# Performance work log

Hardware: AMD Instinct MI355X
Metric: run time of the kernel (lower is better)

## Reference

```python
import jax, jax.numpy as jnp
import numpy as np

N = 50000
E = 600000
HIDDEN = 128
HEADS = 4
HEAD_DIM = HIDDEN // HEADS
NEG_SLOPE = 0.2
LN_EPS = 1e-5


def setup_inputs() -> dict:
    key = jax.random.key(0)
    ks = jax.random.split(key, 16)
    s = 1.0 / np.sqrt(HIDDEN)
    inp = {
        "h": jax.random.normal(ks[0], (N, HIDDEN), dtype=jnp.float32),
        "src": jax.random.randint(ks[1], (E,), 0, N, dtype=jnp.int32),
        "dst": jax.random.randint(ks[2], (E,), 0, N, dtype=jnp.int32),
        # GATv2 params (share_weights=False, bias=True)
        "W_src": jax.random.normal(ks[3], (HIDDEN, HIDDEN), dtype=jnp.float32) * s,
        "b_src": jnp.zeros((HIDDEN,), dtype=jnp.float32),
        "W_dst": jax.random.normal(ks[4], (HIDDEN, HIDDEN), dtype=jnp.float32) * s,
        "b_dst": jnp.zeros((HIDDEN,), dtype=jnp.float32),
        "attn": jax.random.normal(ks[5], (HEADS, HEAD_DIM), dtype=jnp.float32) * s,
        # FFN params
        "W1": jax.random.normal(ks[6], (HIDDEN, 2 * HIDDEN), dtype=jnp.float32) * s,
        "bf1": jnp.zeros((2 * HIDDEN,), dtype=jnp.float32),
        "W2": jax.random.normal(ks[7], (2 * HIDDEN, HIDDEN), dtype=jnp.float32) * (1.0 / np.sqrt(2 * HIDDEN)),
        "bf2": jnp.zeros((HIDDEN,), dtype=jnp.float32),
        # LayerNorms
        "g1": jnp.ones((HIDDEN,), dtype=jnp.float32),
        "beta1": jnp.zeros((HIDDEN,), dtype=jnp.float32),
        "g2": jnp.ones((HIDDEN,), dtype=jnp.float32),
        "beta2": jnp.zeros((HIDDEN,), dtype=jnp.float32),
    }
    return inp


def _layernorm(x, g, b):
    mu = jnp.mean(x, axis=-1, keepdims=True)
    var = jnp.mean(jnp.square(x - mu), axis=-1, keepdims=True)
    return (x - mu) * jax.lax.rsqrt(var + LN_EPS) * g + b


def reference(h, src, dst, W_src, b_src, W_dst, b_dst, attn,
              W1, bf1, W2, bf2, g1, beta1, g2, beta2):
    # --- GATv2 attention (eval mode, dropouts are identity) ---
    fs = (h @ W_src + b_src).reshape(N, HEADS, HEAD_DIM)   # [N,H,D]
    fd = (h @ W_dst + b_dst).reshape(N, HEADS, HEAD_DIM)
    e = jax.nn.leaky_relu(fs[src] + fd[dst], NEG_SLOPE)    # [E,H,D]
    logits = jnp.einsum('ehd,hd->eh', e, attn)             # [E,H]
    # edge softmax over incoming edges of each dst node
    m = jax.ops.segment_max(logits, dst, num_segments=N)   # [N,H]
    m = jnp.where(jnp.isfinite(m), m, 0.0)                 # guard zero-in-degree
    a = jnp.exp(logits - m[dst])                           # [E,H]
    denom = jax.ops.segment_sum(a, dst, num_segments=N)    # [N,H]
    denom = jnp.where(denom == 0.0, 1.0, denom)
    alpha = a / denom[dst]                                 # [E,H]
    msg = fs[src] * alpha[:, :, None]                      # [E,H,D]
    rst = jax.ops.segment_sum(msg, dst, num_segments=N)    # [N,H,D]
    h_attn = rst.reshape(N, HIDDEN)
    # --- residual + LN, FFN + residual + LN ---
    h1 = _layernorm(h + h_attn, g1, beta1)
    ffn = jax.nn.gelu(h1 @ W1 + bf1, approximate=False) @ W2 + bf2
    out = _layernorm(h1 + ffn, g2, beta2)
    return out
```

## Files before the change

kernel.cpp:

```cpp
#include <hip/hip_runtime.h>
#include <math.h>

#define N_NODES 50000
#define N_EDGES 600000
#define HID 128
#define FFN_HID 256
#define NEG_SLOPE 0.2f
#define LN_EPS 1e-5f
#define BKT 64

typedef unsigned short u16;
typedef unsigned int u32;
typedef __attribute__((ext_vector_type(8))) short short8;
typedef __attribute__((ext_vector_type(4))) float floatx4;

__device__ __forceinline__ u16 f2bf(float x) {
    unsigned int u = __float_as_uint(x);
    unsigned int r = u + 0x7FFFu + ((u >> 16) & 1u);
    return (u16)(r >> 16);
}
__device__ __forceinline__ float bflo(u32 u) { return __uint_as_float(u << 16); }
__device__ __forceinline__ float bfhi(u32 u) { return __uint_as_float(u & 0xffff0000u); }
__device__ __forceinline__ u32 packbf(float lo, float hi) {
    return (u32)f2bf(lo) | ((u32)f2bf(hi) << 16);
}


__global__ void scatter_prep(const int* __restrict__ src, const int* __restrict__ dst,
                             int* __restrict__ cursor, u16* __restrict__ ebkt,
                             const float* __restrict__ Wsrc, const float* __restrict__ Wdst,
                             const float* __restrict__ W1, const float* __restrict__ W2,
                             u16* __restrict__ B1, u16* __restrict__ B2, u16* __restrict__ B3) {
    int b = blockIdx.x;
    if (b < 2344) {
        int e = b * 256 + threadIdx.x;
        if (e < N_EDGES) {
            int d = dst[e];
            int slot = atomicAdd(&cursor[d], 1);
            if (slot < BKT) ebkt[(size_t)d * BKT + slot] = (u16)src[e];
        }
        return;
    }
    int t = (b - 2344) * 256 + threadIdx.x;
    const float* W; u16* out; int K, Nc, noff;
    if (t < 16384)       { W = Wsrc; out = B1; K = 128; Nc = 128; noff = 0; }
    else if (t < 32768)  { W = Wdst; out = B1; K = 128; Nc = 128; noff = 128; t -= 16384; }
    else if (t < 65536)  { W = W1;   out = B2; K = 128; Nc = 256; noff = 0;   t -= 32768; }
    else if (t < 98304)  { W = W2;   out = B3; K = 256; Nc = 128; noff = 0;   t -= 65536; }
    else return;
    int n = t % Nc, k = t / Nc;
    int ng = noff + n;
    int ksteps = K >> 5;
    int frag = (ng >> 4) * ksteps + (k >> 5);
    int lane = ((k >> 3) & 3) * 16 + (ng & 15);
    int j = k & 7;
    out[((size_t)frag * 64 + lane) * 8 + j] = f2bf(W[(size_t)k * Nc + n]);
}


__global__ __launch_bounds__(256) void gemm_fsfd_mfma(
    const float* __restrict__ h, const u16* __restrict__ Bsw,
    const float* __restrict__ bsrc, const float* __restrict__ bdst,
    u16* __restrict__ fsb, u16* __restrict__ fdb, u16* __restrict__ hb)
{
    int tid = threadIdx.x, wave = tid >> 6, lane = tid & 63;
    int lrow = lane & 15, lq = lane >> 4;
    short8 bfrag[4][4];
    #pragma unroll
    for (int nt = 0; nt < 4; nt++)
        #pragma unroll
        for (int ks = 0; ks < 4; ks++) {
            int frag = (wave * 4 + nt) * 4 + ks;
            bfrag[nt][ks] = *(const short8*)(Bsw + ((size_t)frag * 64 + lane) * 8);
        }
    float bias[4];
    #pragma unroll
    for (int nt = 0; nt < 4; nt++) {
        int cg = wave * 64 + nt * 16 + lrow;
        bias[nt] = (cg < HID) ? bsrc[cg] : bdst[cg - HID];
    }
    for (int mb = blockIdx.x; mb < N_NODES / 16; mb += gridDim.x) {
        int m0 = mb * 16;
        const float* hrow = h + (size_t)(m0 + lrow) * HID;
        floatx4 acc[4];
        #pragma unroll
        for (int nt = 0; nt < 4; nt++) acc[nt] = {0.f, 0.f, 0.f, 0.f};
        #pragma unroll
        for (int ks = 0; ks < 4; ks++) {
            float4 va = *(const float4*)(hrow + ks * 32 + lq * 8);
            float4 vb = *(const float4*)(hrow + ks * 32 + lq * 8 + 4);
            short8 a;
            a[0] = (short)f2bf(va.x); a[1] = (short)f2bf(va.y);
            a[2] = (short)f2bf(va.z); a[3] = (short)f2bf(va.w);
            a[4] = (short)f2bf(vb.x); a[5] = (short)f2bf(vb.y);
            a[6] = (short)f2bf(vb.z); a[7] = (short)f2bf(vb.w);
            if (wave == 0)
                *(short8*)(hb + (size_t)(m0 + lrow) * HID + ks * 32 + lq * 8) = a;
            #pragma unroll
            for (int nt = 0; nt < 4; nt++)
                acc[nt] = __builtin_amdgcn_mfma_f32_16x16x32_bf16(a, bfrag[nt][ks], acc[nt], 0, 0, 0);
        }
        #pragma unroll
        for (int nt = 0; nt < 4; nt++) {
            int cg = wave * 64 + nt * 16 + lrow;
            u16* outp = (cg < HID) ? (fsb + cg) : (fdb + cg - HID);
            #pragma unroll
            for (int r = 0; r < 4; r++) {
                int row = m0 + lq * 4 + r;
                outp[(size_t)row * HID] = f2bf(acc[nt][r] + bias[nt]);
            }
        }
    }
}


__global__ __launch_bounds__(256) void aggregate_kernel(
    const u16* __restrict__ fsb, const u16* __restrict__ fdb,
    const u16* __restrict__ hb, const float* __restrict__ attn,
    const int* __restrict__ counts, const u16* __restrict__ ebkt,
    const float* __restrict__ g1, const float* __restrict__ beta1,
    u16* __restrict__ h1b)
{
    int wave = threadIdx.x >> 6, lane = threadIdx.x & 63;
    int node = blockIdx.x * 4 + wave;
    if (node >= N_NODES) return;
    int grp = lane >> 4, fl = lane & 15;
    int f = fl * 8;

    uint4 ud = *(const uint4*)&fdb[(size_t)node * HID + f];
    float fdv[8] = { bflo(ud.x), bfhi(ud.x), bflo(ud.y), bfhi(ud.y),
                     bflo(ud.z), bfhi(ud.z), bflo(ud.w), bfhi(ud.w) };
    float4 aA = *(const float4*)&attn[f];
    float4 aB = *(const float4*)&attn[f + 4];
    float c1[8] = { 0.6f * aA.x, 0.6f * aA.y, 0.6f * aA.z, 0.6f * aA.w,
                    0.6f * aB.x, 0.6f * aB.y, 0.6f * aB.z, 0.6f * aB.w };
    float c2[8] = { 0.4f * aA.x, 0.4f * aA.y, 0.4f * aA.z, 0.4f * aA.w,
                    0.4f * aB.x, 0.4f * aB.y, 0.4f * aB.z, 0.4f * aB.w };

    int cnt = counts[node]; cnt = cnt < BKT ? cnt : BKT;
    const u16* brow = ebkt + (size_t)node * BKT;
    float acc[8] = {0.f, 0.f, 0.f, 0.f, 0.f, 0.f, 0.f, 0.f};
    float lsum = 0.f;

    auto body = [&](int e) {
        int s = (int)brow[e];
        uint4 u = *(const uint4*)&fsb[(size_t)s * HID + f];
        float x[8] = { bflo(u.x), bfhi(u.x), bflo(u.y), bfhi(u.y),
                       bflo(u.z), bfhi(u.z), bflo(u.w), bfhi(u.w) };
        float p = 0.f;
        #pragma unroll
        for (int i = 0; i < 8; i++) {
            float ei = x[i] + fdv[i];
            p = fmaf(c1[i], ei, p);
            p = fmaf(c2[i], fabsf(ei), p);
        }
        p += __shfl_xor(p, 1); p += __shfl_xor(p, 2);
        float w = __expf(p);
        lsum += w;
        #pragma unroll
        for (int i = 0; i < 8; i++) acc[i] = fmaf(w, x[i], acc[i]);
    };

    int e = grp;
    for (; e + 4 < cnt; e += 8) { body(e); body(e + 4); }
    if (e < cnt) body(e);

    #pragma unroll
    for (int i = 0; i < 8; i++) {
        acc[i] += __shfl_xor(acc[i], 16);
        acc[i] += __shfl_xor(acc[i], 32);
    }
    lsum += __shfl_xor(lsum, 16); lsum += __shfl_xor(lsum, 32);

    float inv = (lsum > 0.f) ? (1.0f / lsum) : 0.f;
    uint4 uh = *(const uint4*)&hb[(size_t)node * HID + f];
    float hx[8] = { bflo(uh.x), bfhi(uh.x), bflo(uh.y), bfhi(uh.y),
                    bflo(uh.z), bfhi(uh.z), bflo(uh.w), bfhi(uh.w) };
    float o[8], s1 = 0.f, s2 = 0.f;
    #pragma unroll
    for (int i = 0; i < 8; i++) {
        o[i] = hx[i] + acc[i] * inv;
        s1 += o[i]; s2 += o[i] * o[i];
    }
    s1 += __shfl_xor(s1, 1); s2 += __shfl_xor(s2, 1);
    s1 += __shfl_xor(s1, 2); s2 += __shfl_xor(s2, 2);
    s1 += __shfl_xor(s1, 4); s2 += __shfl_xor(s2, 4);
    s1 += __shfl_xor(s1, 8); s2 += __shfl_xor(s2, 8);
    float mu = s1 * (1.0f / HID);
    float var = s2 * (1.0f / HID) - mu * mu;
    float rs = rsqrtf(var + LN_EPS);
    if (grp == 0) {
        float4 gA = *(const float4*)&g1[f], gB = *(const float4*)&g1[f + 4];
        float4 bA = *(const float4*)&beta1[f], bB = *(const float4*)&beta1[f + 4];
        float q0 = (o[0] - mu) * rs * gA.x + bA.x, q1 = (o[1] - mu) * rs * gA.y + bA.y;
        float q2 = (o[2] - mu) * rs * gA.z + bA.z, q3 = (o[3] - mu) * rs * gA.w + bA.w;
        float q4 = (o[4] - mu) * rs * gB.x + bB.x, q5 = (o[5] - mu) * rs * gB.y + bB.y;
        float q6 = (o[6] - mu) * rs * gB.z + bB.z, q7 = (o[7] - mu) * rs * gB.w + bB.w;
        uint4 ob;
        ob.x = packbf(q0, q1); ob.y = packbf(q2, q3);
        ob.z = packbf(q4, q5); ob.w = packbf(q6, q7);
        *(uint4*)&h1b[(size_t)node * HID + f] = ob;
    }
}


#define TS_PAD 8

__global__ __launch_bounds__(256) void ffn_fused(
    const u16* __restrict__ h1b, const u16* __restrict__ B2sw, const u16* __restrict__ B3sw,
    const float* __restrict__ bf1, const float* __restrict__ bf2,
    const float* __restrict__ g2, const float* __restrict__ beta2,
    float* __restrict__ out)
{
    __shared__ u16 ts[16][FFN_HID + TS_PAD];
    __shared__ float xs[16][HID];
    int tid = threadIdx.x, wave = tid >> 6, lane = tid & 63;
    int lrow = lane & 15, lq = lane >> 4;

    short8 b1f[4][4];
    #pragma unroll
    for (int nt = 0; nt < 4; nt++)
        #pragma unroll
        for (int ks = 0; ks < 4; ks++) {
            int frag = (wave * 4 + nt) * 4 + ks;
            b1f[nt][ks] = *(const short8*)(B2sw + ((size_t)frag * 64 + lane) * 8);
        }
    short8 b2f[2][8];
    #pragma unroll
    for (int nt = 0; nt < 2; nt++)
        #pragma unroll
        for (int ks = 0; ks < 8; ks++) {
            int frag = (wave * 2 + nt) * 8 + ks;
            b2f[nt][ks] = *(const short8*)(B3sw + ((size_t)frag * 64 + lane) * 8);
        }
    float bias1[4];
    #pragma unroll
    for (int nt = 0; nt < 4; nt++) bias1[nt] = bf1[wave * 64 + nt * 16 + lrow];
    float bias2[2];
    #pragma unroll
    for (int nt = 0; nt < 2; nt++) bias2[nt] = bf2[wave * 32 + nt * 16 + lrow];

    for (int mb = blockIdx.x; mb < N_NODES / 16; mb += gridDim.x) {
        int m0 = mb * 16;
        floatx4 acc1[4];
        #pragma unroll
        for (int nt = 0; nt < 4; nt++) acc1[nt] = {0.f, 0.f, 0.f, 0.f};
        #pragma unroll
        for (int ks = 0; ks < 4; ks++) {
            short8 a = *(const short8*)(h1b + (size_t)(m0 + lrow) * HID + ks * 32 + lq * 8);
            #pragma unroll
            for (int nt = 0; nt < 4; nt++)
                acc1[nt] = __builtin_amdgcn_mfma_f32_16x16x32_bf16(a, b1f[nt][ks], acc1[nt], 0, 0, 0);
        }
        #pragma unroll
        for (int nt = 0; nt < 4; nt++) {
            int cg = wave * 64 + nt * 16 + lrow;
            #pragma unroll
            for (int r = 0; r < 4; r++) {
                float v = acc1[nt][r] + bias1[nt];
                float ge = v * 0.5f * (1.0f + erff(v * 0.70710678118654752440f));
                ts[lq * 4 + r][cg] = f2bf(ge);
            }
        }
        __syncthreads();
        floatx4 acc2[2];
        #pragma unroll
        for (int nt = 0; nt < 2; nt++) acc2[nt] = {0.f, 0.f, 0.f, 0.f};
        #pragma unroll
        for (int ks = 0; ks < 8; ks++) {
            short8 a = *(const short8*)&ts[lrow][ks * 32 + lq * 8];
            #pragma unroll
            for (int nt = 0; nt < 2; nt++)
                acc2[nt] = __builtin_amdgcn_mfma_f32_16x16x32_bf16(a, b2f[nt][ks], acc2[nt], 0, 0, 0);
        }
        #pragma unroll
        for (int nt = 0; nt < 2; nt++) {
            int cg = wave * 32 + nt * 16 + lrow;
            #pragma unroll
            for (int r = 0; r < 4; r++) {
                int row = m0 + lq * 4 + r;
                float resid = bflo((u32)h1b[(size_t)row * HID + cg] << 0) ;
                resid = __uint_as_float(((u32)h1b[(size_t)row * HID + cg]) << 16);
                xs[lq * 4 + r][cg] = acc2[nt][r] + bias2[nt] + resid;
            }
        }
        __syncthreads();
        int row = tid >> 4, c0 = (tid & 15) * 8;
        float v[8];
        float s1 = 0.f, s2 = 0.f;
        #pragma unroll
        for (int i = 0; i < 8; i++) { v[i] = xs[row][c0 + i]; s1 += v[i]; s2 += v[i] * v[i]; }
        s1 += __shfl_xor(s1, 1); s2 += __shfl_xor(s2, 1);
        s1 += __shfl_xor(s1, 2); s2 += __shfl_xor(s2, 2);
        s1 += __shfl_xor(s1, 4); s2 += __shfl_xor(s2, 4);
        s1 += __shfl_xor(s1, 8); s2 += __shfl_xor(s2, 8);
        float mu = s1 * (1.0f / HID);
        float var = s2 * (1.0f / HID) - mu * mu;
        float rs = rsqrtf(var + LN_EPS);
        float o[8];
        #pragma unroll
        for (int i = 0; i < 8; i++) o[i] = (v[i] - mu) * rs * g2[c0 + i] + beta2[c0 + i];
        float* op = out + (size_t)(m0 + row) * HID + c0;
        *(float4*)(op)     = make_float4(o[0], o[1], o[2], o[3]);
        *(float4*)(op + 4) = make_float4(o[4], o[5], o[6], o[7]);
        __syncthreads();
    }
}


extern "C" void kernel_launch(void* const* d_in, const int* in_sizes, int n_in,
                              void* d_out, int out_size, void* d_ws, size_t ws_size,
                              hipStream_t stream)
{
    const float* h    = (const float*)d_in[0];
    const int*   src  = (const int*)d_in[1];
    const int*   dst  = (const int*)d_in[2];
    const float* Wsrc = (const float*)d_in[3];
    const float* bsrc = (const float*)d_in[4];
    const float* Wdst = (const float*)d_in[5];
    const float* bdst = (const float*)d_in[6];
    const float* attn = (const float*)d_in[7];
    const float* W1   = (const float*)d_in[8];
    const float* bf1  = (const float*)d_in[9];
    const float* W2   = (const float*)d_in[10];
    const float* bf2  = (const float*)d_in[11];
    const float* g1   = (const float*)d_in[12];
    const float* beta1= (const float*)d_in[13];
    const float* g2   = (const float*)d_in[14];
    const float* beta2= (const float*)d_in[15];
    float* out = (float*)d_out;

    u16* fsb = (u16*)d_ws;
    u16* fdb = fsb + (size_t)N_NODES * HID;
    u16* h1b = fdb + (size_t)N_NODES * HID;
    u16* hb  = h1b + (size_t)N_NODES * HID;
    u16* B1 = hb + (size_t)N_NODES * HID;
    u16* B2 = B1 + 32768;
    u16* B3 = B2 + 32768;
    int* cursor = (int*)(B3 + 32768);
    u16* ebkt   = (u16*)(cursor + N_NODES);

    hipMemsetAsync(cursor, 0, N_NODES * sizeof(int), stream);
    scatter_prep<<<2728, 256, 0, stream>>>(src, dst, cursor, ebkt,
                                           Wsrc, Wdst, W1, W2, B1, B2, B3);
    gemm_fsfd_mfma<<<1024, 256, 0, stream>>>(h, B1, bsrc, bdst, fsb, fdb, hb);
    aggregate_kernel<<<(N_NODES + 3) / 4, 256, 0, stream>>>(fsb, fdb, hb, attn, cursor, ebkt, g1, beta1, h1b);
    ffn_fused<<<640, 256, 0, stream>>>(h1b, B2, B3, bf1, bf2, g2, beta2, out);
}
```

Measured before the change: 228.7 us.

## Fuse edge scatter into GEMM launch, drop memset, hoist gathers, use tanh GELU

The memset is folded into the weight-swizzle prep kernel. The edge bucketing scatter now runs as extra blocks inside the fs/fd GEMM launch, which removes one launch and lets the atomics overlap with the MFMA work. The aggregation loop issues both neighbor gathers before computing and splits the dot product into two accumulator chains. The FFN replaces the exact erf GELU with a tanh approximation built on __expf, which changes numerics slightly compared with the exact GELU the reference uses.

```diff
diff --git a/kernel.cpp b/kernel.cpp
--- a/kernel.cpp
+++ b/kernel.cpp
@@ -9,6 +9,9 @@
 #define LN_EPS 1e-5f
 #define BKT 64
 
+#define GEMM_BLOCKS 1024
+#define SCAT_BLOCKS 2344
+
 typedef unsigned short u16;
 typedef unsigned int u32;
 typedef __attribute__((ext_vector_type(8))) short short8;
@@ -26,22 +29,12 @@
 }
 
 
-__global__ void scatter_prep(const int* __restrict__ src, const int* __restrict__ dst,
-                             int* __restrict__ cursor, u16* __restrict__ ebkt,
-                             const float* __restrict__ Wsrc, const float* __restrict__ Wdst,
-                             const float* __restrict__ W1, const float* __restrict__ W2,
-                             u16* __restrict__ B1, u16* __restrict__ B2, u16* __restrict__ B3) {
-    int b = blockIdx.x;
-    if (b < 2344) {
-        int e = b * 256 + threadIdx.x;
-        if (e < N_EDGES) {
-            int d = dst[e];
-            int slot = atomicAdd(&cursor[d], 1);
-            if (slot < BKT) ebkt[(size_t)d * BKT + slot] = (u16)src[e];
-        }
-        return;
-    }
-    int t = (b - 2344) * 256 + threadIdx.x;
+__global__ void prep_zero(const float* __restrict__ Wsrc, const float* __restrict__ Wdst,
+                          const float* __restrict__ W1, const float* __restrict__ W2,
+                          u16* __restrict__ B1, u16* __restrict__ B2, u16* __restrict__ B3,
+                          int* __restrict__ cursor) {
+    int t = blockIdx.x * 256 + threadIdx.x;
+    if (t < N_NODES) cursor[t] = 0;
     const float* W; u16* out; int K, Nc, noff;
     if (t < 16384)       { W = Wsrc; out = B1; K = 128; Nc = 128; noff = 0; }
     else if (t < 32768)  { W = Wdst; out = B1; K = 128; Nc = 128; noff = 128; t -= 16384; }
@@ -58,11 +51,22 @@
 }
 
 
-__global__ __launch_bounds__(256) void gemm_fsfd_mfma(
+__global__ __launch_bounds__(256) void gemm_scatter(
     const float* __restrict__ h, const u16* __restrict__ Bsw,
     const float* __restrict__ bsrc, const float* __restrict__ bdst,
-    u16* __restrict__ fsb, u16* __restrict__ fdb, u16* __restrict__ hb)
+    u16* __restrict__ fsb, u16* __restrict__ fdb, u16* __restrict__ hb,
+    const int* __restrict__ src, const int* __restrict__ dst,
+    int* __restrict__ cursor, u16* __restrict__ ebkt)
 {
+    if (blockIdx.x >= GEMM_BLOCKS) {
+        int e = (blockIdx.x - GEMM_BLOCKS) * 256 + threadIdx.x;
+        if (e < N_EDGES) {
+            int d = dst[e];
+            int slot = atomicAdd(&cursor[d], 1);
+            if (slot < BKT) ebkt[(size_t)d * BKT + slot] = (u16)src[e];
+        }
+        return;
+    }
     int tid = threadIdx.x, wave = tid >> 6, lane = tid & 63;
     int lrow = lane & 15, lq = lane >> 4;
     short8 bfrag[4][4];
@@ -79,7 +83,7 @@
         int cg = wave * 64 + nt * 16 + lrow;
         bias[nt] = (cg < HID) ? bsrc[cg] : bdst[cg - HID];
     }
-    for (int mb = blockIdx.x; mb < N_NODES / 16; mb += gridDim.x) {
+    for (int mb = blockIdx.x; mb < N_NODES / 16; mb += GEMM_BLOCKS) {
         int m0 = mb * 16;
         const float* hrow = h + (size_t)(m0 + lrow) * HID;
         floatx4 acc[4];
@@ -142,18 +146,23 @@
     float acc[8] = {0.f, 0.f, 0.f, 0.f, 0.f, 0.f, 0.f, 0.f};
     float lsum = 0.f;
 
-    auto body = [&](int e) {
-        int s = (int)brow[e];
-        uint4 u = *(const uint4*)&fsb[(size_t)s * HID + f];
+    auto compute = [&](uint4 u) {
         float x[8] = { bflo(u.x), bfhi(u.x), bflo(u.y), bfhi(u.y),
                        bflo(u.z), bfhi(u.z), bflo(u.w), bfhi(u.w) };
-        float p = 0.f;
-        #pragma unroll
-        for (int i = 0; i < 8; i++) {
+        float p0 = 0.f, p1 = 0.f;
+        #pragma unroll
+        for (int i = 0; i < 4; i++) {
             float ei = x[i] + fdv[i];
-            p = fmaf(c1[i], ei, p);
-            p = fmaf(c2[i], fabsf(ei), p);
-        }
+            p0 = fmaf(c1[i], ei, p0);
+            p0 = fmaf(c2[i], fabsf(ei), p0);
+        }
+        #pragma unroll
+        for (int i = 4; i < 8; i++) {
+            float ei = x[i] + fdv[i];
+            p1 = fmaf(c1[i], ei, p1);
+            p1 = fmaf(c2[i], fabsf(ei), p1);
+        }
+        float p = p0 + p1;
         p += __shfl_xor(p, 1); p += __shfl_xor(p, 2);
         float w = __expf(p);
         lsum += w;
@@ -162,8 +171,17 @@
     };
 
     int e = grp;
-    for (; e + 4 < cnt; e += 8) { body(e); body(e + 4); }
-    if (e < cnt) body(e);
+    for (; e + 4 < cnt; e += 8) {
+        int sA = (int)brow[e], sB = (int)brow[e + 4];
+        uint4 uA = *(const uint4*)&fsb[(size_t)sA * HID + f];
+        uint4 uB = *(const uint4*)&fsb[(size_t)sB * HID + f];
+        compute(uA);
+        compute(uB);
+    }
+    if (e < cnt) {
+        int s = (int)brow[e];
+        compute(*(const uint4*)&fsb[(size_t)s * HID + f]);
+    }
 
     #pragma unroll
     for (int i = 0; i < 8; i++) {
@@ -206,6 +224,14 @@
 
 #define TS_PAD 8
 
+__device__ __forceinline__ float gelu_fast(float v) {
+    float y = 0.7978845608f * (v + 0.044715f * v * v * v);
+    y = fminf(fmaxf(y, -15.f), 15.f);
+    float z = __expf(2.f * y);
+    float th = (z - 1.f) / (z + 1.f);
+    return 0.5f * v * (1.f + th);
+}
+
 __global__ __launch_bounds__(256) void ffn_fused(
     const u16* __restrict__ h1b, const u16* __restrict__ B2sw, const u16* __restrict__ B3sw,
     const float* __restrict__ bf1, const float* __restrict__ bf2,
@@ -258,8 +284,7 @@
             #pragma unroll
             for (int r = 0; r < 4; r++) {
                 float v = acc1[nt][r] + bias1[nt];
-                float ge = v * 0.5f * (1.0f + erff(v * 0.70710678118654752440f));
-                ts[lq * 4 + r][cg] = f2bf(ge);
+                ts[lq * 4 + r][cg] = f2bf(gelu_fast(v));
             }
         }
         __syncthreads();
@@ -279,8 +304,7 @@
             #pragma unroll
             for (int r = 0; r < 4; r++) {
                 int row = m0 + lq * 4 + r;
-                float resid = bflo((u32)h1b[(size_t)row * HID + cg] << 0) ;
-                resid = __uint_as_float(((u32)h1b[(size_t)row * HID + cg]) << 16);
+                float resid = __uint_as_float(((u32)h1b[(size_t)row * HID + cg]) << 16);
                 xs[lq * 4 + r][cg] = acc2[nt][r] + bias2[nt] + resid;
             }
         }
@@ -340,10 +364,9 @@
     int* cursor = (int*)(B3 + 32768);
     u16* ebkt   = (u16*)(cursor + N_NODES);
 
-    hipMemsetAsync(cursor, 0, N_NODES * sizeof(int), stream);
-    scatter_prep<<<2728, 256, 0, stream>>>(src, dst, cursor, ebkt,
-                                           Wsrc, Wdst, W1, W2, B1, B2, B3);
-    gemm_fsfd_mfma<<<1024, 256, 0, stream>>>(h, B1, bsrc, bdst, fsb, fdb, hb);
+    prep_zero<<<384, 256, 0, stream>>>(Wsrc, Wdst, W1, W2, B1, B2, B3, cursor);
+    gemm_scatter<<<GEMM_BLOCKS + SCAT_BLOCKS, 256, 0, stream>>>(
+        h, B1, bsrc, bdst, fsb, fdb, hb, src, dst, cursor, ebkt);
     aggregate_kernel<<<(N_NODES + 3) / 4, 256, 0, stream>>>(fsb, fdb, hb, attn, cursor, ebkt, g1, beta1, h1b);
     ffn_fused<<<640, 256, 0, stream>>>(h1b, B2, B3, bf1, bf2, g2, beta2, out);
 }
```

Result: slower. 248.6 us (+8.7%).
